# Performance work log

Measured on AMD Instinct MI355X. Metric: run time of the kernel, lower is better.

## Reference

```python
import jax, jax.numpy as jnp
import numpy as np

GROUPS = 32
EPS = 1e-5
N_HEADS = 8


def setup_inputs() -> dict:
    key = jax.random.key(0)
    ks = jax.random.split(key, 12)
    B, H, W, C = 16, 64, 64, 512
    Nctx, Dctx = 77, 768
    s_c = 1.0 / np.sqrt(C)
    s_ctx = 1.0 / np.sqrt(Dctx)
    return {
        "x": jax.random.normal(ks[0], (B, H, W, C), jnp.float32),
        "context": jax.random.normal(ks[1], (B, Nctx, Dctx), jnp.float32),
        "gn_scale": jnp.ones((C,), jnp.float32),
        "gn_bias": jnp.zeros((C,), jnp.float32),
        "wq": jax.random.normal(ks[2], (C, C), jnp.float32) * s_c,
        "bq": jnp.zeros((C,), jnp.float32),
        "wk": jax.random.normal(ks[3], (Dctx, C), jnp.float32) * s_ctx,
        "bk": jnp.zeros((C,), jnp.float32),
        "wv": jax.random.normal(ks[4], (Dctx, C), jnp.float32) * s_ctx,
        "bv": jnp.zeros((C,), jnp.float32),
        "wo": jax.random.normal(ks[5], (C, C), jnp.float32) * s_c,
        "bo": jnp.zeros((C,), jnp.float32),
    }


def _group_norm(x, scale, bias):
    B, H, W, C = x.shape
    xg = x.reshape(B, H, W, GROUPS, C // GROUPS)
    mean = jnp.mean(xg, axis=(1, 2, 4), keepdims=True)
    var = jnp.var(xg, axis=(1, 2, 4), keepdims=True)
    xn = (xg - mean) * jax.lax.rsqrt(var + EPS)
    return xn.reshape(B, H, W, C) * scale + bias


def reference(x, context, gn_scale, gn_bias, wq, bq, wk, bk, wv, bv, wo, bo):
    B, H, W, C = x.shape
    head_dim = C // N_HEADS
    h = _group_norm(x, gn_scale, gn_bias)
    h_flat = h.reshape(B, H * W, C)
    Q = h_flat @ wq + bq                      # [B, N, C]
    K = context @ wk + bk                     # [B, Nctx, C]
    V = context @ wv + bv

    def split_heads(t):
        b, n, c = t.shape
        return t.reshape(b, n, N_HEADS, head_dim).transpose(0, 2, 1, 3)

    Qh, Kh, Vh = split_heads(Q), split_heads(K), split_heads(V)
    scale = 1.0 / jnp.sqrt(jnp.asarray(head_dim, x.dtype))
    scores = jnp.einsum('bhid,bhjd->bhij', Qh, Kh) * scale
    attn = jax.nn.softmax(scores, axis=-1)
    out = jnp.einsum('bhij,bhjd->bhid', attn, Vh)  # [B, h, N, d]
    out = out.transpose(0, 2, 1, 3).reshape(B, H * W, C)
    out = out @ wo + bo
    return out.reshape(B, H, W, C) + x
```

## Files before the change

### kernel.cpp

```cpp
#include <hip/hip_runtime.h>
#include <hip/hip_bf16.h>

typedef __attribute__((ext_vector_type(4))) float f32x4;
typedef __attribute__((ext_vector_type(8))) short bf16x8;
typedef unsigned short u16;

#define AS1 __attribute__((address_space(1)))
#define AS3 __attribute__((address_space(3)))

#define B_    16
#define HW_   4096
#define C_    512
#define NCTX  77
#define DCTX  768
#define NH    8
#define HD    64
#define EPSV  1e-5f

__device__ inline u16 f2bf(float f) {
    union { float f; unsigned u; } v; v.f = f;
    unsigned r = v.u + 0x7fffu + ((v.u >> 16) & 1u);
    return (u16)(r >> 16);
}
__device__ inline float bf2f(u16 h) {
    union { unsigned u; float f; } v; v.u = ((unsigned)h) << 16;
    return v.f;
}

__global__ __launch_bounds__(256) void gn_stats(const float* __restrict__ x,
                                                float* __restrict__ mean,
                                                float* __restrict__ rstd) {
    int b = blockIdx.x >> 5, g = blockIdx.x & 31;
    const float* px = x + (size_t)b * HW_ * C_ + g * 16;
    float s = 0.f, ss = 0.f;
    for (int t = threadIdx.x; t < HW_ * 4; t += 256) {
        int hw = t >> 2, c4 = (t & 3) * 4;
        const float4 v = *(const float4*)(px + (size_t)hw * C_ + c4);
        s  += v.x + v.y + v.z + v.w;
        ss += v.x * v.x + v.y * v.y + v.z * v.z + v.w * v.w;
    }
    for (int off = 32; off; off >>= 1) { s += __shfl_xor(s, off); ss += __shfl_xor(ss, off); }
    __shared__ float red[2][4];
    int wv = threadIdx.x >> 6, lane = threadIdx.x & 63;
    if (lane == 0) { red[0][wv] = s; red[1][wv] = ss; }
    __syncthreads();
    if (threadIdx.x == 0) {
        float S = red[0][0] + red[0][1] + red[0][2] + red[0][3];
        float SS = red[1][0] + red[1][1] + red[1][2] + red[1][3];
        float mn = S / 65536.f;
        float var = SS / 65536.f - mn * mn;
        mean[blockIdx.x] = mn;
        rstd[blockIdx.x] = rsqrtf(var + EPSV);
    }
}

__global__ __launch_bounds__(256) void cast_ctx(const float* __restrict__ src,
                                                u16* __restrict__ dst, int n4) {
    int i = blockIdx.x * 256 + threadIdx.x;
    if (i >= n4) return;
    float4 v = *(const float4*)(src + (size_t)i * 4);
    ushort4 o;
    o.x = f2bf(v.x); o.y = f2bf(v.y); o.z = f2bf(v.z); o.w = f2bf(v.w);
    *(ushort4*)(dst + (size_t)i * 4) = o;
}

__global__ __launch_bounds__(256) void transpose_cast(const float* __restrict__ src,
                                                      u16* __restrict__ dst, int K) {
    int idx = blockIdx.x * 256 + threadIdx.x;
    if (idx >= K * 512) return;
    int k = idx >> 9, n = idx & 511;
    dst[(size_t)n * K + k] = f2bf(src[idx]);
}

__global__ __launch_bounds__(256) void gemm_small(const u16* __restrict__ A,
                                                  const u16* __restrict__ Bt,
                                                  const float* __restrict__ bias,
                                                  u16* __restrict__ out,
                                                  int M, int K) {
    __shared__ __align__(16) u16 As[128][40];
    __shared__ __align__(16) u16 Bs[128][40];
    int tid = threadIdx.x, lane = tid & 63, wid = tid >> 6;
    int wm = wid >> 1, wn = wid & 1;
    int row0 = blockIdx.y * 128, col0 = blockIdx.x * 128;
    int q = lane >> 4, r16 = lane & 15;

    f32x4 acc[4][4];
#pragma unroll
    for (int i = 0; i < 4; i++)
#pragma unroll
        for (int j = 0; j < 4; j++) acc[i][j] = (f32x4){0.f, 0.f, 0.f, 0.f};

    for (int k0 = 0; k0 < K; k0 += 32) {
#pragma unroll
        for (int it = 0; it < 2; ++it) {
            int e = it * 256 + tid;
            int rr = e >> 2, kc = (e & 3) * 8;
            int ga = row0 + rr; if (ga > M - 1) ga = M - 1;
            bf16x8 av = *(const bf16x8*)(A + (size_t)ga * K + k0 + kc);
            *(bf16x8*)&As[rr][kc] = av;
            int gb = col0 + rr;
            bf16x8 bv = *(const bf16x8*)(Bt + (size_t)gb * K + k0 + kc);
            *(bf16x8*)&Bs[rr][kc] = bv;
        }
        __syncthreads();
        bf16x8 afr[4], bfr[4];
#pragma unroll
        for (int mi = 0; mi < 4; mi++) afr[mi] = *(const bf16x8*)&As[wm * 64 + mi * 16 + r16][q * 8];
#pragma unroll
        for (int ni = 0; ni < 4; ni++) bfr[ni] = *(const bf16x8*)&Bs[wn * 64 + ni * 16 + r16][q * 8];
#pragma unroll
        for (int mi = 0; mi < 4; mi++)
#pragma unroll
            for (int ni = 0; ni < 4; ni++)
                acc[mi][ni] = __builtin_amdgcn_mfma_f32_16x16x32_bf16(afr[mi], bfr[ni], acc[mi][ni], 0, 0, 0);
        __syncthreads();
    }

#pragma unroll
    for (int mi = 0; mi < 4; mi++) {
#pragma unroll
        for (int rr = 0; rr < 4; rr++) {
            int grow = row0 + wm * 64 + mi * 16 + q * 4 + rr;
            if (grow >= M) continue;
#pragma unroll
            for (int ni = 0; ni < 4; ni++) {
                int gcol = col0 + wn * 64 + ni * 16 + r16;
                float v = acc[mi][ni][rr] + bias[gcol];
                out[(size_t)grow * 512 + gcol] = f2bf(v);
            }
        }
    }
}

__global__ __launch_bounds__(256, 2) void gemm_fusedq(const float* __restrict__ x,
                                                      const float* __restrict__ mean,
                                                      const float* __restrict__ rstd,
                                                      const float* __restrict__ gns,
                                                      const float* __restrict__ gnb,
                                                      const u16* __restrict__ Bt,
                                                      const float* __restrict__ bias,
                                                      u16* __restrict__ out) {
    constexpr int K = 512;
    __shared__ __align__(16) u16 LA[2][8192];
    __shared__ __align__(16) u16 LB[2][8192];
    int tid = threadIdx.x, lane = tid & 63, wid = tid >> 6;
    int wr = wid >> 1, wc = wid & 1;
    int q = lane >> 4, r16 = lane & 15;

    int orig = blockIdx.x;
    int wg = (orig & 7) * 256 + (orig >> 3);
    int bx = wg & 3, by = wg >> 2;
    int row0 = by * 128, col0 = bx * 128;

    int srow = tid >> 3;
    int schunk = (tid & 7) ^ (srow & 7);
    const u16* gB = Bt + (size_t)(col0 + srow) * K + schunk * 8;
    const int lo = tid * 8;

    int c8 = tid & 7;
    int rbase = (tid >> 3) * 4;
    const float* xb = x + (size_t)(row0 + rbase) * 512 + c8 * 8;
    int bg0 = (row0 >> 12) * 32;

    f32x4 acc[4][4];
#pragma unroll
    for (int i = 0; i < 4; i++)
#pragma unroll
        for (int j = 0; j < 4; j++) acc[i][j] = (f32x4){0.f, 0.f, 0.f, 0.f};

    float4 ar[8];
    float mn, rs;
    float4 s0v, s1v, b0v, b1v;

#define LOADA(kt) do { _Pragma("unroll")                                          \
    for (int i_ = 0; i_ < 4; ++i_) {                                              \
        ar[2 * i_]     = *(const float4*)(xb + (kt) * 64 + (size_t)i_ * 512);     \
        ar[2 * i_ + 1] = *(const float4*)(xb + (kt) * 64 + (size_t)i_ * 512 + 4); \
    } } while (0)

#define LOADP(kt) do { int c0_ = (kt) * 64 + c8 * 8; int bg_ = bg0 + (c0_ >> 4);  \
    mn = mean[bg_]; rs = rstd[bg_];                                               \
    s0v = *(const float4*)(gns + c0_); s1v = *(const float4*)(gns + c0_ + 4);     \
    b0v = *(const float4*)(gnb + c0_); b1v = *(const float4*)(gnb + c0_ + 4);     \
  } while (0)

#define WRITEA(nbuf) do {                                                         \
    float m2_[8], a2_[8];                                                         \
    m2_[0]=rs*s0v.x; m2_[1]=rs*s0v.y; m2_[2]=rs*s0v.z; m2_[3]=rs*s0v.w;           \
    m2_[4]=rs*s1v.x; m2_[5]=rs*s1v.y; m2_[6]=rs*s1v.z; m2_[7]=rs*s1v.w;           \
    a2_[0]=b0v.x-mn*m2_[0]; a2_[1]=b0v.y-mn*m2_[1];                               \
    a2_[2]=b0v.z-mn*m2_[2]; a2_[3]=b0v.w-mn*m2_[3];                               \
    a2_[4]=b1v.x-mn*m2_[4]; a2_[5]=b1v.y-mn*m2_[5];                               \
    a2_[6]=b1v.z-mn*m2_[6]; a2_[7]=b1v.w-mn*m2_[7];                               \
    _Pragma("unroll")                                                             \
    for (int i_ = 0; i_ < 4; ++i_) {                                              \
        int row_ = rbase + i_;                                                    \
        bf16x8 pk_;                                                               \
        pk_[0]=(short)f2bf(ar[2*i_].x  *m2_[0]+a2_[0]);                           \
        pk_[1]=(short)f2bf(ar[2*i_].y  *m2_[1]+a2_[1]);                           \
        pk_[2]=(short)f2bf(ar[2*i_].z  *m2_[2]+a2_[2]);                           \
        pk_[3]=(short)f2bf(ar[2*i_].w  *m2_[3]+a2_[3]);                           \
        pk_[4]=(short)f2bf(ar[2*i_+1].x*m2_[4]+a2_[4]);                           \
        pk_[5]=(short)f2bf(ar[2*i_+1].y*m2_[5]+a2_[5]);                           \
        pk_[6]=(short)f2bf(ar[2*i_+1].z*m2_[6]+a2_[6]);                           \
        pk_[7]=(short)f2bf(ar[2*i_+1].w*m2_[7]+a2_[7]);                           \
        *(bf16x8*)&LA[nbuf][row_ * 64 + ((c8 ^ (row_ & 7)) * 8)] = pk_;           \
    } } while (0)

#define STG_B(kt, s) __builtin_amdgcn_global_load_lds( \
        (const AS1 void*)(gB + (kt) * 64 + (size_t)((s) * 32) * K), \
        (AS3 void*)(&LB[(kt) & 1][(s) * 2048 + lo]), 16, 0, 0)

#define PHASE_(buf, h, ks) do {                                                            \
    bf16x8 afr[2], bfr[4];                                                                 \
    const int ch_ = (((ks) * 4 + q) ^ (r16 & 7)) * 8;                                      \
    _Pragma("unroll")                                                                      \
    for (int mi = 0; mi < 2; mi++)                                                         \
        afr[mi] = *(const bf16x8*)&LA[buf][(wr * 64 + ((h) * 2 + mi) * 16 + r16) * 64 + ch_]; \
    _Pragma("unroll")                                                                      \
    for (int ni = 0; ni < 4; ni++)                                                         \
        bfr[ni] = *(const bf16x8*)&LB[buf][(wc * 64 + ni * 16 + r16) * 64 + ch_];          \
    __builtin_amdgcn_s_setprio(1);                                                         \
    _Pragma("unroll")                                                                      \
    for (int mi = 0; mi < 2; mi++)                                                         \
      _Pragma("unroll")                                                                    \
      for (int ni = 0; ni < 4; ni++)                                                       \
        acc[(h) * 2 + mi][ni] =                                                            \
            __builtin_amdgcn_mfma_f32_16x16x32_bf16(afr[mi], bfr[ni], acc[(h) * 2 + mi][ni], 0, 0, 0); \
    __builtin_amdgcn_s_setprio(0);                                                         \
  } while (0)

    LOADA(0); LOADP(0);
    asm volatile("" ::: "memory");
    STG_B(0, 0); STG_B(0, 1); STG_B(0, 2); STG_B(0, 3);
    asm volatile("s_waitcnt vmcnt(4)" ::: "memory");
    WRITEA(0);
    asm volatile("s_waitcnt lgkmcnt(0)" ::: "memory");

#pragma unroll
    for (int t = 0; t < 7; ++t) {
        const int buf = t & 1;
        LOADA(t + 1); LOADP(t + 1);
        asm volatile("" ::: "memory");
        STG_B(t + 1, 0); STG_B(t + 1, 1); STG_B(t + 1, 2); STG_B(t + 1, 3);
        asm volatile("s_waitcnt vmcnt(18)" ::: "memory");
        __builtin_amdgcn_s_barrier();
        asm volatile("" ::: "memory");
        PHASE_(buf, 0, 0); PHASE_(buf, 1, 0); PHASE_(buf, 0, 1); PHASE_(buf, 1, 1);
        asm volatile("s_waitcnt vmcnt(4)" ::: "memory");
        WRITEA(buf ^ 1);
        asm volatile("s_waitcnt lgkmcnt(0)" ::: "memory");
        __builtin_amdgcn_s_barrier();
        asm volatile("" ::: "memory");
    }
    asm volatile("s_waitcnt vmcnt(0) lgkmcnt(0)" ::: "memory");
    __builtin_amdgcn_s_barrier();
    asm volatile("" ::: "memory");
    PHASE_(1, 0, 0); PHASE_(1, 1, 0); PHASE_(1, 0, 1); PHASE_(1, 1, 1);
#undef LOADA
#undef LOADP
#undef WRITEA
#undef STG_B
#undef PHASE_

#pragma unroll
    for (int mi = 0; mi < 4; mi++) {
#pragma unroll
        for (int rr = 0; rr < 4; rr++) {
            int grow = row0 + wr * 64 + mi * 16 + q * 4 + rr;
#pragma unroll
            for (int ni = 0; ni < 4; ni++) {
                int gcol = col0 + wc * 64 + ni * 16 + r16;
                float v = acc[mi][ni][rr] + bias[gcol];
                out[(size_t)grow * 512 + gcol] = f2bf(v);
            }
        }
    }
}

template <int EPI>
__global__ __launch_bounds__(256, 2) void gemm_big(const u16* __restrict__ A,
                                                   const u16* __restrict__ Bt,
                                                   const float* __restrict__ bias,
                                                   const float* __restrict__ res,
                                                   void* __restrict__ out) {
    constexpr int K = 512;
    __shared__ __align__(16) u16 LA[2][8192];
    __shared__ __align__(16) u16 LB[2][8192];
    int tid = threadIdx.x, lane = tid & 63, wid = tid >> 6;
    int wr = wid >> 1, wc = wid & 1;
    int q = lane >> 4, r16 = lane & 15;

    int orig = blockIdx.x;
    int wg = (orig & 7) * 256 + (orig >> 3);
    int bx = wg & 3, by = wg >> 2;
    int row0 = by * 128, col0 = bx * 128;

    int srow = tid >> 3;
    int schunk = (tid & 7) ^ (srow & 7);
    const u16* gA = A + (size_t)(row0 + srow) * K + schunk * 8;
    const u16* gB = Bt + (size_t)(col0 + srow) * K + schunk * 8;
    const int lo = tid * 8;

    f32x4 acc[4][4];
#pragma unroll
    for (int i = 0; i < 4; i++)
#pragma unroll
        for (int j = 0; j < 4; j++) acc[i][j] = (f32x4){0.f, 0.f, 0.f, 0.f};

#define STG_A(kt, s) __builtin_amdgcn_global_load_lds( \
        (const AS1 void*)(gA + (kt) * 64 + (size_t)((s) * 32) * K), \
        (AS3 void*)(&LA[(kt) & 1][(s) * 2048 + lo]), 16, 0, 0)
#define STG_B(kt, s) __builtin_amdgcn_global_load_lds( \
        (const AS1 void*)(gB + (kt) * 64 + (size_t)((s) * 32) * K), \
        (AS3 void*)(&LB[(kt) & 1][(s) * 2048 + lo]), 16, 0, 0)

#define PHASE_(buf, h, ks) do {                                                            \
    bf16x8 afr[2], bfr[4];                                                                 \
    const int ch_ = (((ks) * 4 + q) ^ (r16 & 7)) * 8;                                      \
    _Pragma("unroll")                                                                      \
    for (int mi = 0; mi < 2; mi++)                                                         \
        afr[mi] = *(const bf16x8*)&LA[buf][(wr * 64 + ((h) * 2 + mi) * 16 + r16) * 64 + ch_]; \
    _Pragma("unroll")                                                                      \
    for (int ni = 0; ni < 4; ni++)                                                         \
        bfr[ni] = *(const bf16x8*)&LB[buf][(wc * 64 + ni * 16 + r16) * 64 + ch_];          \
    __builtin_amdgcn_s_setprio(1);                                                         \
    _Pragma("unroll")                                                                      \
    for (int mi = 0; mi < 2; mi++)                                                         \
      _Pragma("unroll")                                                                    \
      for (int ni = 0; ni < 4; ni++)                                                       \
        acc[(h) * 2 + mi][ni] =                                                            \
            __builtin_amdgcn_mfma_f32_16x16x32_bf16(afr[mi], bfr[ni], acc[(h) * 2 + mi][ni], 0, 0, 0); \
    __builtin_amdgcn_s_setprio(0);                                                         \
  } while (0)

    STG_A(0, 0); STG_A(0, 1); STG_A(0, 2); STG_A(0, 3);
    STG_B(0, 0); STG_B(0, 1); STG_B(0, 2); STG_B(0, 3);
    for (int t = 0; t < 7; ++t) {
        const int buf = t & 1;
        STG_A(t + 1, 0); STG_A(t + 1, 1);
        asm volatile("s_waitcnt vmcnt(2)" ::: "memory");
        __builtin_amdgcn_s_barrier();
        asm volatile("" ::: "memory");
        PHASE_(buf, 0, 0);
        asm volatile("" ::: "memory");
        STG_A(t + 1, 2); STG_A(t + 1, 3);
        PHASE_(buf, 1, 0);
        asm volatile("" ::: "memory");
        STG_B(t + 1, 0); STG_B(t + 1, 1);
        PHASE_(buf, 0, 1);
        asm volatile("" ::: "memory");
        STG_B(t + 1, 2); STG_B(t + 1, 3);
        PHASE_(buf, 1, 1);
        asm volatile("" ::: "memory");
        __builtin_amdgcn_s_barrier();
    }
    asm volatile("s_waitcnt vmcnt(0)" ::: "memory");
    __builtin_amdgcn_s_barrier();
    asm volatile("" ::: "memory");
    PHASE_(1, 0, 0); PHASE_(1, 1, 0); PHASE_(1, 0, 1); PHASE_(1, 1, 1);
#undef STG_A
#undef STG_B
#undef PHASE_

#pragma unroll
    for (int mi = 0; mi < 4; mi++) {
#pragma unroll
        for (int rr = 0; rr < 4; rr++) {
            int grow = row0 + wr * 64 + mi * 16 + q * 4 + rr;
#pragma unroll
            for (int ni = 0; ni < 4; ni++) {
                int gcol = col0 + wc * 64 + ni * 16 + r16;
                float v = acc[mi][ni][rr] + bias[gcol];
                size_t idx = (size_t)grow * 512 + gcol;
                if (EPI == 0) ((u16*)out)[idx] = f2bf(v);
                else          ((float*)out)[idx] = v + res[idx];
            }
        }
    }
}

__global__ __launch_bounds__(256) void attn_mfma(const u16* __restrict__ Qb,
                                                 const u16* __restrict__ Kb,
                                                 const u16* __restrict__ Vb,
                                                 u16* __restrict__ Ob) {
    __shared__ __align__(16) u16 Ks[80][72];
    __shared__ __align__(16) u16 VT[64][104];
    __shared__ __align__(16) u16 Ps[64][104];
    int tid = threadIdx.x, lane = tid & 63, wv = tid >> 6;
    int q = lane >> 4, r16 = lane & 15;
    int tile0 = blockIdx.x * 16;
    int bh = blockIdx.y;
    int b = bh >> 3, h = bh & 7;

    {
        unsigned* p0 = (unsigned*)&Ks[0][0];
        for (int i = tid; i < 2880; i += 256) p0[i] = 0u;
        unsigned* p1 = (unsigned*)&VT[0][0];
        for (int i = tid; i < 3328; i += 256) p1[i] = 0u;
        unsigned* p2 = (unsigned*)&Ps[0][0];
        for (int i = tid; i < 3328; i += 256) p2[i] = 0u;
    }
    __syncthreads();

    size_t kvbase = ((size_t)b * NCTX) * C_ + h * HD;
    for (int c = tid; c < NCTX * 8; c += 256) {
        int j = c >> 3, d8 = (c & 7) * 8;
        *(bf16x8*)&Ks[j][d8] = *(const bf16x8*)(Kb + kvbase + (size_t)j * C_ + d8);
    }
    for (int t = tid; t < NCTX * 64; t += 256) {
        int j = t >> 6, d = t & 63;
        VT[d][j] = Vb[kvbase + (size_t)j * C_ + d];
    }
    __syncthreads();

    const size_t tstep = (size_t)64 * C_;
    const u16* qp = Qb + ((size_t)b * HW_ + wv * 16 + r16) * C_ + h * HD + q * 8;
    bool v4 = (r16 < NCTX - 64);

    bf16x8 qc0 = *(const bf16x8*)(qp + (size_t)tile0 * tstep);
    bf16x8 qc1 = *(const bf16x8*)(qp + (size_t)tile0 * tstep + 32);

    for (int it = 0; it < 16; ++it) {
        int tile = tile0 + it;
        bf16x8 qn0 = qc0, qn1 = qc1;
        if (it < 15) {
            qn0 = *(const bf16x8*)(qp + (size_t)(tile + 1) * tstep);
            qn1 = *(const bf16x8*)(qp + (size_t)(tile + 1) * tstep + 32);
        }

        f32x4 accs[5];
#pragma unroll
        for (int nt = 0; nt < 5; ++nt) accs[nt] = (f32x4){0.f, 0.f, 0.f, 0.f};
#pragma unroll
        for (int nt = 0; nt < 5; ++nt) {
            bf16x8 kf = *(const bf16x8*)&Ks[nt * 16 + r16][q * 8];
            accs[nt] = __builtin_amdgcn_mfma_f32_16x16x32_bf16(qc0, kf, accs[nt], 0, 0, 0);
        }
#pragma unroll
        for (int nt = 0; nt < 5; ++nt) {
            bf16x8 kf = *(const bf16x8*)&Ks[nt * 16 + r16][32 + q * 8];
            accs[nt] = __builtin_amdgcn_mfma_f32_16x16x32_bf16(qc1, kf, accs[nt], 0, 0, 0);
        }

#pragma unroll
        for (int r = 0; r < 4; ++r) {
            float s[5];
#pragma unroll
            for (int nt = 0; nt < 5; ++nt) s[nt] = accs[nt][r] * 0.125f;
            float m = fmaxf(fmaxf(fmaxf(s[0], s[1]), fmaxf(s[2], s[3])), v4 ? s[4] : -3.0e38f);
#pragma unroll
            for (int off = 1; off < 16; off <<= 1) m = fmaxf(m, __shfl_xor(m, off));
            float e[5], sum = 0.f;
#pragma unroll
            for (int nt = 0; nt < 5; ++nt) {
                e[nt] = (nt < 4 || v4) ? __expf(s[nt] - m) : 0.f;
                sum += e[nt];
            }
#pragma unroll
            for (int off = 1; off < 16; off <<= 1) sum += __shfl_xor(sum, off);
            float inv = 1.0f / sum;
            int prow = wv * 16 + q * 4 + r;
#pragma unroll
            for (int nt = 0; nt < 5; ++nt)
                Ps[prow][nt * 16 + r16] = f2bf(e[nt] * inv);
        }

        f32x4 acco[4];
#pragma unroll
        for (int nt = 0; nt < 4; ++nt) acco[nt] = (f32x4){0.f, 0.f, 0.f, 0.f};
#pragma unroll
        for (int ks = 0; ks < 3; ++ks) {
            bf16x8 pf = *(const bf16x8*)&Ps[wv * 16 + r16][ks * 32 + q * 8];
#pragma unroll
            for (int nt = 0; nt < 4; ++nt) {
                bf16x8 vf = *(const bf16x8*)&VT[nt * 16 + r16][ks * 32 + q * 8];
                acco[nt] = __builtin_amdgcn_mfma_f32_16x16x32_bf16(pf, vf, acco[nt], 0, 0, 0);
            }
        }

        int row0 = tile * 64 + wv * 16;
#pragma unroll
        for (int nt = 0; nt < 4; ++nt)
#pragma unroll
            for (int r = 0; r < 4; ++r) {
                int row = row0 + q * 4 + r;
                int col = h * HD + nt * 16 + r16;
                Ob[((size_t)b * HW_ + row) * C_ + col] = f2bf(acco[nt][r]);
            }
        qc0 = qn0; qc1 = qn1;
    }
}

extern "C" void kernel_launch(void* const* d_in, const int* in_sizes, int n_in,
                              void* d_out, int out_size, void* d_ws, size_t ws_size,
                              hipStream_t stream) {
    const float* x   = (const float*)d_in[0];
    const float* ctx = (const float*)d_in[1];
    const float* gns = (const float*)d_in[2];
    const float* gnb = (const float*)d_in[3];
    const float* wq  = (const float*)d_in[4];
    const float* bq  = (const float*)d_in[5];
    const float* wk  = (const float*)d_in[6];
    const float* bk  = (const float*)d_in[7];
    const float* wv  = (const float*)d_in[8];
    const float* bv  = (const float*)d_in[9];
    const float* wo  = (const float*)d_in[10];
    const float* bo  = (const float*)d_in[11];

    char* ws = (char*)d_ws;
    float* mean = (float*)(ws + 0);
    float* rstd = (float*)(ws + 2048);
    u16* wqT  = (u16*)(ws + 4096);
    u16* wkT  = (u16*)(ws + 528384);
    u16* wvT  = (u16*)(ws + 1314816);
    u16* woT  = (u16*)(ws + 2101248);
    u16* ctxb = (u16*)(ws + 2625536);
    u16* aob  = (u16*)(ws + 4517888);
    u16* qb   = (u16*)(ws + 71626752);
    u16* kb   = (u16*)(ws + 138735616);
    u16* vb   = (u16*)(ws + 139997184);

    gn_stats<<<512, 256, 0, stream>>>(x, mean, rstd);
    cast_ctx<<<924, 256, 0, stream>>>(ctx, ctxb, 236544);
    transpose_cast<<<1024, 256, 0, stream>>>(wq, wqT, 512);
    transpose_cast<<<1536, 256, 0, stream>>>(wk, wkT, 768);
    transpose_cast<<<1536, 256, 0, stream>>>(wv, wvT, 768);
    transpose_cast<<<1024, 256, 0, stream>>>(wo, woT, 512);

    gemm_fusedq<<<2048, 256, 0, stream>>>(x, mean, rstd, gns, gnb, wqT, bq, qb);
    gemm_small<<<dim3(4, 10), 256, 0, stream>>>(ctxb, wkT, bk, kb, 1232, 768);
    gemm_small<<<dim3(4, 10), 256, 0, stream>>>(ctxb, wvT, bv, vb, 1232, 768);

    attn_mfma<<<dim3(4, 128), 256, 0, stream>>>(qb, kb, vb, aob);

    gemm_big<1><<<2048, 256, 0, stream>>>(aob, woT, bo, x, d_out);
}
```

Measured before the change: 314.8 us.

## Replace double-buffered output GEMM with 4-slot ring pipeline; fuse context cast into K/V GEMMs

The output-projection GEMM changes from a 2-stage, 64-wide K double buffer to a 4-slot ring of 32-wide K tiles. It keeps three tiles in flight, with one barrier per step, and the whole loop is unrolled. Separately, the context fp32-to-bf16 cast kernel is removed and the K/V small GEMMs convert fp32 context on load. The aim is better latency hiding in the big GEMM and one less launch and memory pass, at the cost of more barriers per K and redundant casts across column blocks.

```diff
diff --git a/kernel.cpp b/kernel.cpp
--- a/kernel.cpp
+++ b/kernel.cpp
@@ -54,16 +54,6 @@
     }
 }
 
-__global__ __launch_bounds__(256) void cast_ctx(const float* __restrict__ src,
-                                                u16* __restrict__ dst, int n4) {
-    int i = blockIdx.x * 256 + threadIdx.x;
-    if (i >= n4) return;
-    float4 v = *(const float4*)(src + (size_t)i * 4);
-    ushort4 o;
-    o.x = f2bf(v.x); o.y = f2bf(v.y); o.z = f2bf(v.z); o.w = f2bf(v.w);
-    *(ushort4*)(dst + (size_t)i * 4) = o;
-}
-
 __global__ __launch_bounds__(256) void transpose_cast(const float* __restrict__ src,
                                                       u16* __restrict__ dst, int K) {
     int idx = blockIdx.x * 256 + threadIdx.x;
@@ -72,7 +62,7 @@
     dst[(size_t)n * K + k] = f2bf(src[idx]);
 }
 
-__global__ __launch_bounds__(256) void gemm_small(const u16* __restrict__ A,
+__global__ __launch_bounds__(256) void gemm_small(const float* __restrict__ A,
                                                   const u16* __restrict__ Bt,
                                                   const float* __restrict__ bias,
                                                   u16* __restrict__ out,
@@ -96,7 +86,13 @@
             int e = it * 256 + tid;
             int rr = e >> 2, kc = (e & 3) * 8;
             int ga = row0 + rr; if (ga > M - 1) ga = M - 1;
-            bf16x8 av = *(const bf16x8*)(A + (size_t)ga * K + k0 + kc);
+            float4 a0 = *(const float4*)(A + (size_t)ga * K + k0 + kc);
+            float4 a1 = *(const float4*)(A + (size_t)ga * K + k0 + kc + 4);
+            bf16x8 av;
+            av[0] = (short)f2bf(a0.x); av[1] = (short)f2bf(a0.y);
+            av[2] = (short)f2bf(a0.z); av[3] = (short)f2bf(a0.w);
+            av[4] = (short)f2bf(a1.x); av[5] = (short)f2bf(a1.y);
+            av[6] = (short)f2bf(a1.z); av[7] = (short)f2bf(a1.w);
             *(bf16x8*)&As[rr][kc] = av;
             int gb = col0 + rr;
             bf16x8 bv = *(const bf16x8*)(Bt + (size_t)gb * K + k0 + kc);
@@ -278,15 +274,14 @@
     }
 }
 
-template <int EPI>
-__global__ __launch_bounds__(256, 2) void gemm_big(const u16* __restrict__ A,
-                                                   const u16* __restrict__ Bt,
-                                                   const float* __restrict__ bias,
-                                                   const float* __restrict__ res,
-                                                   void* __restrict__ out) {
+__global__ __launch_bounds__(256, 2) void gemm_ring(const u16* __restrict__ A,
+                                                    const u16* __restrict__ Bt,
+                                                    const float* __restrict__ bias,
+                                                    const float* __restrict__ res,
+                                                    float* __restrict__ out) {
     constexpr int K = 512;
-    __shared__ __align__(16) u16 LA[2][8192];
-    __shared__ __align__(16) u16 LB[2][8192];
+    __shared__ __align__(16) u16 LA[4][4096];
+    __shared__ __align__(16) u16 LB[4][4096];
     int tid = threadIdx.x, lane = tid & 63, wid = tid >> 6;
     int wr = wid >> 1, wc = wid & 1;
     int q = lane >> 4, r16 = lane & 15;
@@ -296,8 +291,8 @@
     int bx = wg & 3, by = wg >> 2;
     int row0 = by * 128, col0 = bx * 128;
 
-    int srow = tid >> 3;
-    int schunk = (tid & 7) ^ (srow & 7);
+    int srow = tid >> 2;
+    int schunk = (tid & 3) ^ (srow & 3);
     const u16* gA = A + (size_t)(row0 + srow) * K + schunk * 8;
     const u16* gB = Bt + (size_t)(col0 + srow) * K + schunk * 8;
     const int lo = tid * 8;
@@ -308,60 +303,54 @@
 #pragma unroll
         for (int j = 0; j < 4; j++) acc[i][j] = (f32x4){0.f, 0.f, 0.f, 0.f};
 
-#define STG_A(kt, s) __builtin_amdgcn_global_load_lds( \
-        (const AS1 void*)(gA + (kt) * 64 + (size_t)((s) * 32) * K), \
-        (AS3 void*)(&LA[(kt) & 1][(s) * 2048 + lo]), 16, 0, 0)
-#define STG_B(kt, s) __builtin_amdgcn_global_load_lds( \
-        (const AS1 void*)(gB + (kt) * 64 + (size_t)((s) * 32) * K), \
-        (AS3 void*)(&LB[(kt) & 1][(s) * 2048 + lo]), 16, 0, 0)
-
-#define PHASE_(buf, h, ks) do {                                                            \
-    bf16x8 afr[2], bfr[4];                                                                 \
-    const int ch_ = (((ks) * 4 + q) ^ (r16 & 7)) * 8;                                      \
-    _Pragma("unroll")                                                                      \
-    for (int mi = 0; mi < 2; mi++)                                                         \
-        afr[mi] = *(const bf16x8*)&LA[buf][(wr * 64 + ((h) * 2 + mi) * 16 + r16) * 64 + ch_]; \
-    _Pragma("unroll")                                                                      \
-    for (int ni = 0; ni < 4; ni++)                                                         \
-        bfr[ni] = *(const bf16x8*)&LB[buf][(wc * 64 + ni * 16 + r16) * 64 + ch_];          \
-    __builtin_amdgcn_s_setprio(1);                                                         \
-    _Pragma("unroll")                                                                      \
-    for (int mi = 0; mi < 2; mi++)                                                         \
-      _Pragma("unroll")                                                                    \
-      for (int ni = 0; ni < 4; ni++)                                                       \
-        acc[(h) * 2 + mi][ni] =                                                            \
-            __builtin_amdgcn_mfma_f32_16x16x32_bf16(afr[mi], bfr[ni], acc[(h) * 2 + mi][ni], 0, 0, 0); \
-    __builtin_amdgcn_s_setprio(0);                                                         \
+#define STG(kt) do { int sl_ = (kt) & 3;                                              \
+    __builtin_amdgcn_global_load_lds((const AS1 void*)(gA + (kt) * 32),               \
+                                     (AS3 void*)(&LA[sl_][lo]), 16, 0, 0);            \
+    __builtin_amdgcn_global_load_lds((const AS1 void*)(gA + (kt) * 32 + (size_t)64 * K), \
+                                     (AS3 void*)(&LA[sl_][2048 + lo]), 16, 0, 0);     \
+    __builtin_amdgcn_global_load_lds((const AS1 void*)(gB + (kt) * 32),               \
+                                     (AS3 void*)(&LB[sl_][lo]), 16, 0, 0);            \
+    __builtin_amdgcn_global_load_lds((const AS1 void*)(gB + (kt) * 32 + (size_t)64 * K), \
+                                     (AS3 void*)(&LB[sl_][2048 + lo]), 16, 0, 0);     \
   } while (0)
 
-    STG_A(0, 0); STG_A(0, 1); STG_A(0, 2); STG_A(0, 3);
-    STG_B(0, 0); STG_B(0, 1); STG_B(0, 2); STG_B(0, 3);
-    for (int t = 0; t < 7; ++t) {
-        const int buf = t & 1;
-        STG_A(t + 1, 0); STG_A(t + 1, 1);
-        asm volatile("s_waitcnt vmcnt(2)" ::: "memory");
-        __builtin_amdgcn_s_barrier();
-        asm volatile("" ::: "memory");
-        PHASE_(buf, 0, 0);
-        asm volatile("" ::: "memory");
-        STG_A(t + 1, 2); STG_A(t + 1, 3);
-        PHASE_(buf, 1, 0);
-        asm volatile("" ::: "memory");
-        STG_B(t + 1, 0); STG_B(t + 1, 1);
-        PHASE_(buf, 0, 1);
-        asm volatile("" ::: "memory");
-        STG_B(t + 1, 2); STG_B(t + 1, 3);
-        PHASE_(buf, 1, 1);
-        asm volatile("" ::: "memory");
-        __builtin_amdgcn_s_barrier();
-    }
+#define COMPUTE(sl) do {                                                              \
+    bf16x8 afr[4], bfr[4];                                                            \
+    const int ch_ = (q ^ (r16 & 3)) * 8;                                              \
+    _Pragma("unroll")                                                                 \
+    for (int mi = 0; mi < 4; mi++)                                                    \
+        afr[mi] = *(const bf16x8*)&LA[sl][(wr * 64 + mi * 16 + r16) * 32 + ch_];      \
+    _Pragma("unroll")                                                                 \
+    for (int ni = 0; ni < 4; ni++)                                                    \
+        bfr[ni] = *(const bf16x8*)&LB[sl][(wc * 64 + ni * 16 + r16) * 32 + ch_];      \
+    __builtin_amdgcn_s_setprio(1);                                                    \
+    _Pragma("unroll")                                                                 \
+    for (int mi = 0; mi < 4; mi++)                                                    \
+      _Pragma("unroll")                                                               \
+      for (int ni = 0; ni < 4; ni++)                                                  \
+        acc[mi][ni] = __builtin_amdgcn_mfma_f32_16x16x32_bf16(afr[mi], bfr[ni], acc[mi][ni], 0, 0, 0); \
+    __builtin_amdgcn_s_setprio(0);                                                    \
+  } while (0)
+
+    STG(0); STG(1); STG(2);
+#pragma unroll
+    for (int t = 0; t < 13; ++t) {
+        asm volatile("s_waitcnt vmcnt(8)" ::: "memory");
+        asm volatile("s_barrier" ::: "memory");
+        COMPUTE(t & 3);
+        STG(t + 3);
+    }
+    asm volatile("s_waitcnt vmcnt(8)" ::: "memory");
+    asm volatile("s_barrier" ::: "memory");
+    COMPUTE(1);
+    asm volatile("s_waitcnt vmcnt(4)" ::: "memory");
+    asm volatile("s_barrier" ::: "memory");
+    COMPUTE(2);
     asm volatile("s_waitcnt vmcnt(0)" ::: "memory");
-    __builtin_amdgcn_s_barrier();
-    asm volatile("" ::: "memory");
-    PHASE_(1, 0, 0); PHASE_(1, 1, 0); PHASE_(1, 0, 1); PHASE_(1, 1, 1);
-#undef STG_A
-#undef STG_B
-#undef PHASE_
+    asm volatile("s_barrier" ::: "memory");
+    COMPUTE(3);
+#undef STG
+#undef COMPUTE
 
 #pragma unroll
     for (int mi = 0; mi < 4; mi++) {
@@ -373,8 +362,7 @@
                 int gcol = col0 + wc * 64 + ni * 16 + r16;
                 float v = acc[mi][ni][rr] + bias[gcol];
                 size_t idx = (size_t)grow * 512 + gcol;
-                if (EPI == 0) ((u16*)out)[idx] = f2bf(v);
-                else          ((float*)out)[idx] = v + res[idx];
+                out[idx] = v + res[idx];
             }
         }
     }
@@ -515,24 +503,22 @@
     u16* wkT  = (u16*)(ws + 528384);
     u16* wvT  = (u16*)(ws + 1314816);
     u16* woT  = (u16*)(ws + 2101248);
-    u16* ctxb = (u16*)(ws + 2625536);
     u16* aob  = (u16*)(ws + 4517888);
     u16* qb   = (u16*)(ws + 71626752);
     u16* kb   = (u16*)(ws + 138735616);
     u16* vb   = (u16*)(ws + 139997184);
 
     gn_stats<<<512, 256, 0, stream>>>(x, mean, rstd);
-    cast_ctx<<<924, 256, 0, stream>>>(ctx, ctxb, 236544);
     transpose_cast<<<1024, 256, 0, stream>>>(wq, wqT, 512);
     transpose_cast<<<1536, 256, 0, stream>>>(wk, wkT, 768);
     transpose_cast<<<1536, 256, 0, stream>>>(wv, wvT, 768);
     transpose_cast<<<1024, 256, 0, stream>>>(wo, woT, 512);
 
     gemm_fusedq<<<2048, 256, 0, stream>>>(x, mean, rstd, gns, gnb, wqT, bq, qb);
-    gemm_small<<<dim3(4, 10), 256, 0, stream>>>(ctxb, wkT, bk, kb, 1232, 768);
-    gemm_small<<<dim3(4, 10), 256, 0, stream>>>(ctxb, wvT, bv, vb, 1232, 768);
+    gemm_small<<<dim3(4, 10), 256, 0, stream>>>(ctx, wkT, bk, kb, 1232, 768);
+    gemm_small<<<dim3(4, 10), 256, 0, stream>>>(ctx, wvT, bv, vb, 1232, 768);
 
     attn_mfma<<<dim3(4, 128), 256, 0, stream>>>(qb, kb, vb, aob);
 
-    gemm_big<1><<<2048, 256, 0, stream>>>(aob, woT, bo, x, d_out);
-}
+    gemm_ring<<<2048, 256, 0, stream>>>(aob, woT, bo, x, (float*)d_out);
+}
```

Measured after the change: 323.7 us. 2.8% more time.
